# Kernel optimization log

Hardware: AMD Instinct MI355X
Metric: run time of the kernel (lower is better)

## Reference

```python
import jax, jax.numpy as jnp
import numpy as np

B, C, H, W = 16, 512, 64, 64
R = 8
CP = C // R  # inner channel dim C' = 64


def setup_inputs() -> dict:
    key = jax.random.key(0)
    ks = jax.random.split(key, 10)
    s_in = 1.0 / np.sqrt(C)
    s_cp = 1.0 / np.sqrt(CP)
    return {
        "x": jax.random.normal(ks[0], (B, C, H, W), dtype=jnp.float32),
        "wq": jax.random.uniform(ks[1], (CP, C), jnp.float32, -s_in, s_in),
        "bq": jax.random.uniform(ks[2], (CP,), jnp.float32, -s_in, s_in),
        "wk": jax.random.uniform(ks[3], (CP, C), jnp.float32, -s_in, s_in),
        "bk": jax.random.uniform(ks[4], (CP,), jnp.float32, -s_in, s_in),
        "wv": jax.random.uniform(ks[5], (CP, C), jnp.float32, -s_in, s_in),
        "bv": jax.random.uniform(ks[6], (CP,), jnp.float32, -s_in, s_in),
        "wo": jax.random.uniform(ks[7], (C, CP), jnp.float32, -s_cp, s_cp),
        "bo": jax.random.uniform(ks[8], (C,), jnp.float32, -s_cp, s_cp),
        # torch init is gamma=0 (output==x, zero grads to convs); use small
        # nonzero value so the reference exercises the full graph.
        "gamma": jax.random.normal(ks[9], (1,), dtype=jnp.float32) * 0.1,
    }


def reference(x, wq, bq, wk, bk, wv, bv, wo, bo, gamma):
    b, c, h, w = x.shape
    n = h * w
    xf = x.reshape(b, c, n)  # flatten spatial -> (B, C, N)
    # 1x1 convs == channel matmuls
    q = jnp.einsum("oc,bcn->bon", wq, xf) + bq[:, None]  # (B, C', N)
    k = jnp.einsum("oc,bcn->bon", wk, xf) + bk[:, None]  # (B, C', N)
    v = jnp.einsum("oc,bcn->bon", wv, xf) + bv[:, None]  # (B, C', N)
    # energy = bmm(key (B,C',N), query^T (B,N,C')) -> (B, C', C')
    energy = jnp.einsum("bin,bjn->bij", k, q)
    attention = jax.nn.softmax(energy, axis=-1)  # (B, C', C')
    out = jnp.einsum("bij,bjn->bin", attention, v)  # (B, C', N)
    out = jnp.einsum("co,bon->bcn", wo, out) + bo[:, None]  # (B, C, N)
    out = out.reshape(b, c, h, w)
    return gamma * out + x
```

## Files before the change

kernel.cpp:

```cpp
#include <hip/hip_runtime.h>


#define NN 4096
#define CIN 512
#define CPD 64

typedef short s8v __attribute__((ext_vector_type(8)));
typedef float f4v __attribute__((ext_vector_type(4)));
typedef unsigned short u16;

__device__ __forceinline__ u16 f2bf(float f) {
    union { float f; unsigned int u; } c; c.f = f;
    unsigned int r = c.u + 0x7FFFu + ((c.u >> 16) & 1u);
    return (u16)(r >> 16);
}

union PK { uint2 u[2]; s8v v; };

__global__ __launch_bounds__(256) void k_prep(
    const float* __restrict__ wq, const float* __restrict__ wk,
    const float* __restrict__ wv, const float* __restrict__ wo,
    u16* __restrict__ wqkvb, u16* __restrict__ wob)
{
    const int t = blockIdx.x * 256 + threadIdx.x;
    const int i4 = t * 4;
    const float* src; u16* dst; int off;
    if (i4 < 98304) {
        const int r = i4 >> 15;
        src = (r == 0) ? wq : (r == 1) ? wk : wv;
        off = i4 & 32767;
        dst = wqkvb + (r << 15);
    } else {
        src = wo; off = i4 - 98304; dst = wob;
    }
    float4 v = *(const float4*)(src + off);
    u16 tmp[4] = { f2bf(v.x), f2bf(v.y), f2bf(v.z), f2bf(v.w) };
    *(uint2*)(dst + off) = *(const uint2*)tmp;
}

__global__ __launch_bounds__(256, 4) void k_qkv(
    const float* __restrict__ x, const u16* __restrict__ wqkvb,
    const float* __restrict__ bq, const float* __restrict__ bk,
    const float* __restrict__ bv,
    u16* __restrict__ q, u16* __restrict__ k, u16* __restrict__ vt)
{
    const int nb = blockIdx.x, b = blockIdx.y;
    const int t = threadIdx.x;
    const int w = t >> 6, L = t & 63, quad = L >> 4, l15 = L & 15;
    const int n0 = nb * 64;

    __shared__ u16 xs[2][64 * 64];

    const int nl = t & 63, c4b = t >> 6;
    const float* xp = x + (size_t)b * CIN * NN + n0 + nl;

    f4v acc[3][4];
    #pragma unroll
    for (int p = 0; p < 3; ++p)
        #pragma unroll
        for (int nn = 0; nn < 4; ++nn) acc[p][nn] = (f4v){0.f,0.f,0.f,0.f};

    const u16* wb = wqkvb + (size_t)(w * 16 + l15) * CIN;

    float xr[16];
    #pragma unroll
    for (int i = 0; i < 4; ++i)
        #pragma unroll
        for (int j = 0; j < 4; ++j)
            xr[i * 4 + j] = xp[(size_t)((c4b + 4 * i) * 4 + j) * NN];
    #pragma unroll
    for (int i = 0; i < 4; ++i) {
        u16 t4[4];
        #pragma unroll
        for (int j = 0; j < 4; ++j) t4[j] = f2bf(xr[i * 4 + j]);
        const int slot = (c4b + 4 * i) ^ (nl & 15);
        *(uint2*)&xs[0][nl * 64 + slot * 4] = *(const uint2*)t4;
    }
    __syncthreads();

    for (int cc = 0; cc < 8; ++cc) {
        const int buf = cc & 1;
        if (cc < 7) {
            const int c0n = (cc + 1) * 64;
            #pragma unroll
            for (int i = 0; i < 4; ++i)
                #pragma unroll
                for (int j = 0; j < 4; ++j)
                    xr[i * 4 + j] = xp[(size_t)(c0n + (c4b + 4 * i) * 4 + j) * NN];
        }
        #pragma unroll
        for (int ks2 = 0; ks2 < 2; ++ks2) {
            s8v bf[4];
            #pragma unroll
            for (int nn = 0; nn < 4; ++nn) {
                const int row = nn * 16 + l15;
                const int sb = ks2 * 8 + quad * 2;
                PK p_;
                p_.u[0] = *(const uint2*)&xs[buf][row * 64 + ((sb ^ l15) * 4)];
                p_.u[1] = *(const uint2*)&xs[buf][row * 64 + (((sb + 1) ^ l15) * 4)];
                bf[nn] = p_.v;
            }
            const int cgl = cc * 64 + ks2 * 32 + quad * 8;
            #pragma unroll
            for (int p = 0; p < 3; ++p) {
                s8v af = *(const s8v*)(wb + (size_t)p * 64 * CIN + cgl);
                #pragma unroll
                for (int nn = 0; nn < 4; ++nn)
                    acc[p][nn] = __builtin_amdgcn_mfma_f32_16x16x32_bf16(
                        af, bf[nn], acc[p][nn], 0, 0, 0);
            }
        }
        if (cc < 7) {
            #pragma unroll
            for (int i = 0; i < 4; ++i) {
                u16 t4[4];
                #pragma unroll
                for (int j = 0; j < 4; ++j) t4[j] = f2bf(xr[i * 4 + j]);
                const int slot = (c4b + 4 * i) ^ (nl & 15);
                *(uint2*)&xs[buf ^ 1][nl * 64 + slot * 4] = *(const uint2*)t4;
            }
        }
        __syncthreads();
    }

    const int orow = w * 16 + quad * 4;
    {
        float4 q4 = *(const float4*)(bq + orow);
        float4 k4 = *(const float4*)(bk + orow);
        const float qb_[4] = { q4.x, q4.y, q4.z, q4.w };
        const float kb_[4] = { k4.x, k4.y, k4.z, k4.w };
        u16* qp = q + (size_t)b * CPD * NN;
        u16* kp = k + (size_t)b * CPD * NN;
        #pragma unroll
        for (int nn = 0; nn < 4; ++nn) {
            const int n = n0 + nn * 16 + l15;
            #pragma unroll
            for (int r = 0; r < 4; ++r) {
                qp[(size_t)(orow + r) * NN + n] = f2bf(acc[0][nn][r] + qb_[r]);
                kp[(size_t)(orow + r) * NN + n] = f2bf(acc[1][nn][r] + kb_[r]);
            }
        }
    }
    {
        float4 v4 = *(const float4*)(bv + orow);
        const float vb_[4] = { v4.x, v4.y, v4.z, v4.w };
        u16* vtb = vt + (size_t)b * NN * CPD;
        #pragma unroll
        for (int nn = 0; nn < 4; ++nn) {
            const int n = n0 + nn * 16 + l15;
            u16 tmp[4];
            #pragma unroll
            for (int r = 0; r < 4; ++r) tmp[r] = f2bf(acc[2][nn][r] + vb_[r]);
            *(uint2*)(vtb + (size_t)n * CPD + orow) = *(const uint2*)tmp;
        }
    }
}

__global__ __launch_bounds__(256, 4) void k_energy(
    const u16* __restrict__ q, const u16* __restrict__ k,
    float* __restrict__ epart)
{
    const int s = blockIdx.x;
    const int b = blockIdx.y;
    const int t = threadIdx.x;
    const int wv_ = t >> 6, L = t & 63, quad = L >> 4, l15 = L & 15;
    const u16* kb = k + (size_t)b * CPD * NN;
    const u16* qb = q + (size_t)b * CPD * NN;

    f4v acc[4][4];
    #pragma unroll
    for (int a = 0; a < 4; ++a)
        #pragma unroll
        for (int d = 0; d < 4; ++d) acc[a][d] = (f4v){0.f,0.f,0.f,0.f};

    const int nbase = s * 512 + wv_ * 128;
    #pragma unroll
    for (int ksl = 0; ksl < 4; ++ksl) {
        const int n = nbase + ksl * 32 + quad * 8;
        s8v af[4], bf_[4];
        #pragma unroll
        for (int it = 0; it < 4; ++it)
            af[it] = *(const s8v*)(kb + (size_t)(it * 16 + l15) * NN + n);
        #pragma unroll
        for (int jt = 0; jt < 4; ++jt)
            bf_[jt] = *(const s8v*)(qb + (size_t)(jt * 16 + l15) * NN + n);
        #pragma unroll
        for (int it = 0; it < 4; ++it)
            #pragma unroll
            for (int jt = 0; jt < 4; ++jt)
                acc[it][jt] = __builtin_amdgcn_mfma_f32_16x16x32_bf16(
                    af[it], bf_[jt], acc[it][jt], 0, 0, 0);
    }

    float* ep = epart + ((size_t)b * 32 + s * 4 + wv_) * 4096;
    #pragma unroll
    for (int it = 0; it < 4; ++it)
        #pragma unroll
        for (int jt = 0; jt < 4; ++jt)
            #pragma unroll
            for (int r = 0; r < 4; ++r)
                ep[(it * 16 + quad * 4 + r) * 64 + jt * 16 + l15] =
                    acc[it][jt][r];
}

__global__ __launch_bounds__(64) void k_softmax(
    const float* __restrict__ epart, u16* __restrict__ attn)
{
    const int i = blockIdx.x;
    const int b = blockIdx.y;
    const int j = threadIdx.x;
    float s = 0.f;
    #pragma unroll
    for (int sp = 0; sp < 32; ++sp)
        s += epart[((size_t)b * 32 + sp) * 4096 + i * 64 + j];
    float m = s;
    #pragma unroll
    for (int off = 32; off; off >>= 1) m = fmaxf(m, __shfl_xor(m, off));
    float e = __expf(s - m);
    float tot = e;
    #pragma unroll
    for (int off = 32; off; off >>= 1) tot += __shfl_xor(tot, off);
    attn[(size_t)b * 4096 + i * 64 + j] = f2bf(e / tot);
}

__global__ __launch_bounds__(256, 4) void k_avout(
    const u16* __restrict__ vt, const u16* __restrict__ attn,
    const u16* __restrict__ wob, const float* __restrict__ bo,
    const float* __restrict__ gamma, const float* __restrict__ x,
    float* __restrict__ out)
{
    const int nb = blockIdx.x, b = blockIdx.y;
    const int t = threadIdx.x;
    const int wv_ = t >> 6, L = t & 63, quad = L >> 4, l15 = L & 15;
    const int n0 = nb * 64;

    __shared__ u16 avl[64 * 64];

    {
        const u16* ab  = attn + (size_t)b * 4096;
        const u16* vtb = vt + (size_t)b * NN * CPD;
        f4v acc1[4];
        #pragma unroll
        for (int a = 0; a < 4; ++a) acc1[a] = (f4v){0.f,0.f,0.f,0.f};
        const int nloc = wv_ * 16 + l15;
        #pragma unroll
        for (int ks = 0; ks < 2; ++ks) {
            const int j = ks * 32 + quad * 8;
            s8v bfv = *(const s8v*)(vtb + (size_t)(n0 + nloc) * CPD + j);
            #pragma unroll
            for (int it = 0; it < 4; ++it) {
                s8v af = *(const s8v*)(ab + (size_t)(it * 16 + l15) * 64 + j);
                acc1[it] = __builtin_amdgcn_mfma_f32_16x16x32_bf16(
                    af, bfv, acc1[it], 0, 0, 0);
            }
        }
        #pragma unroll
        for (int it = 0; it < 4; ++it) {
            u16 t4[4];
            #pragma unroll
            for (int r = 0; r < 4; ++r) t4[r] = f2bf(acc1[it][r]);
            const int slot = (it * 4 + quad) ^ l15;
            *(uint2*)&avl[nloc * 64 + slot * 4] = *(const uint2*)t4;
        }
    }
    __syncthreads();

    const float g = gamma[0];
    for (int cb = 0; cb < 8; ++cb) {
        f4v acc2[4];
        #pragma unroll
        for (int a = 0; a < 4; ++a) acc2[a] = (f4v){0.f,0.f,0.f,0.f};
        #pragma unroll
        for (int ks = 0; ks < 2; ++ks) {
            const int sb = ks * 8 + quad * 2;
            PK p_;
            p_.u[0] = *(const uint2*)&avl[(wv_ * 16 + l15) * 64 + ((sb ^ l15) * 4)];
            p_.u[1] = *(const uint2*)&avl[(wv_ * 16 + l15) * 64 + (((sb + 1) ^ l15) * 4)];
            const s8v af2 = p_.v;
            const int i0 = ks * 32 + quad * 8;
            #pragma unroll
            for (int ct = 0; ct < 4; ++ct) {
                s8v bf2 = *(const s8v*)(wob +
                    (size_t)(cb * 64 + ct * 16 + l15) * CPD + i0);
                acc2[ct] = __builtin_amdgcn_mfma_f32_16x16x32_bf16(
                    af2, bf2, acc2[ct], 0, 0, 0);
            }
        }
        #pragma unroll
        for (int ct = 0; ct < 4; ++ct) {
            const int c = cb * 64 + ct * 16 + l15;
            const float bs = bo[c];
            const int nb4 = n0 + wv_ * 16 + quad * 4;
            const size_t idx = ((size_t)b * CIN + c) * NN + nb4;
            float4 xr = *(const float4*)(x + idx);
            float4 r4;
            r4.x = g * (acc2[ct][0] + bs) + xr.x;
            r4.y = g * (acc2[ct][1] + bs) + xr.y;
            r4.z = g * (acc2[ct][2] + bs) + xr.z;
            r4.w = g * (acc2[ct][3] + bs) + xr.w;
            *(float4*)(out + idx) = r4;
        }
    }
}

extern "C" void kernel_launch(void* const* d_in, const int* in_sizes, int n_in,
                              void* d_out, int out_size, void* d_ws, size_t ws_size,
                              hipStream_t stream) {
    const float* x  = (const float*)d_in[0];
    const float* wq = (const float*)d_in[1];
    const float* bq = (const float*)d_in[2];
    const float* wk = (const float*)d_in[3];
    const float* bk = (const float*)d_in[4];
    const float* wv = (const float*)d_in[5];
    const float* bv = (const float*)d_in[6];
    const float* wo = (const float*)d_in[7];
    const float* bo = (const float*)d_in[8];
    const float* gm = (const float*)d_in[9];
    float* out = (float*)d_out;

    char* wsb = (char*)d_ws;
    u16*   q     = (u16*)wsb;
    u16*   k     = (u16*)(wsb + 8388608);
    u16*   vt    = (u16*)(wsb + 16777216);
    float* epart = (float*)(wsb + 25165824);
    u16*   attn  = (u16*)(wsb + 33554432);
    u16*   wqkvb = (u16*)(wsb + 33685504);
    u16*   wob   = (u16*)(wsb + 33882112);

    k_prep<<<128, 256, 0, stream>>>(wq, wk, wv, wo, wqkvb, wob);
    k_qkv<<<dim3(64, 16), 256, 0, stream>>>(x, wqkvb, bq, bk, bv, q, k, vt);
    k_energy<<<dim3(8, 16), 256, 0, stream>>>(q, k, epart);
    k_softmax<<<dim3(64, 16), 64, 0, stream>>>(epart, attn);
    k_avout<<<dim3(64, 16), 256, 0, stream>>>(vt, attn, wob, bo, gm, x, out);
}
```

Baseline: 346.6 us.

## Fuse energy computation into QKV kernel via LDS-staged Q/K tiles

The per-tile Q and K results now go into shared memory instead of global memory, and each QKV block computes its partial 64x64 energy directly, writing 64 partials per batch. This removes the separate energy kernel and the global write and re-read of Q and K. The price is twice as much partial-energy traffic, which the softmax kernel must sum over more slices. The x loads in QKV are also software-pipelined two chunks ahead with two register buffers, and the x residual loads in the output kernel are hoisted ahead of the MFMAs.

Measured after the change: 347.4 us. About the same (+0.2%).

```diff
diff --git a/kernel.cpp b/kernel.cpp
--- a/kernel.cpp
+++ b/kernel.cpp
@@ -38,11 +38,11 @@
     *(uint2*)(dst + off) = *(const uint2*)tmp;
 }
 
-__global__ __launch_bounds__(256, 4) void k_qkv(
+__global__ __launch_bounds__(256, 4) void k_qkve(
     const float* __restrict__ x, const u16* __restrict__ wqkvb,
     const float* __restrict__ bq, const float* __restrict__ bk,
     const float* __restrict__ bv,
-    u16* __restrict__ q, u16* __restrict__ k, u16* __restrict__ vt)
+    u16* __restrict__ vt, float* __restrict__ epart)
 {
     const int nb = blockIdx.x, b = blockIdx.y;
     const int t = threadIdx.x;
@@ -62,32 +62,27 @@
 
     const u16* wb = wqkvb + (size_t)(w * 16 + l15) * CIN;
 
-    float xr[16];
-    #pragma unroll
-    for (int i = 0; i < 4; ++i)
-        #pragma unroll
-        for (int j = 0; j < 4; ++j)
-            xr[i * 4 + j] = xp[(size_t)((c4b + 4 * i) * 4 + j) * NN];
-    #pragma unroll
-    for (int i = 0; i < 4; ++i) {
-        u16 t4[4];
-        #pragma unroll
-        for (int j = 0; j < 4; ++j) t4[j] = f2bf(xr[i * 4 + j]);
-        const int slot = (c4b + 4 * i) ^ (nl & 15);
-        *(uint2*)&xs[0][nl * 64 + slot * 4] = *(const uint2*)t4;
-    }
-    __syncthreads();
-
-    for (int cc = 0; cc < 8; ++cc) {
-        const int buf = cc & 1;
-        if (cc < 7) {
-            const int c0n = (cc + 1) * 64;
-            #pragma unroll
-            for (int i = 0; i < 4; ++i)
-                #pragma unroll
-                for (int j = 0; j < 4; ++j)
-                    xr[i * 4 + j] = xp[(size_t)(c0n + (c4b + 4 * i) * 4 + j) * NN];
-        }
+    float xrA[16], xrB[16];
+
+    auto issue = [&](int cc, float* xr) {
+        const int c0n = cc * 64;
+        #pragma unroll
+        for (int i = 0; i < 4; ++i)
+            #pragma unroll
+            for (int j = 0; j < 4; ++j)
+                xr[i * 4 + j] = xp[(size_t)(c0n + (c4b + 4 * i) * 4 + j) * NN];
+    };
+    auto stage = [&](const float* xr, u16* dst) {
+        #pragma unroll
+        for (int i = 0; i < 4; ++i) {
+            u16 t4[4];
+            #pragma unroll
+            for (int j = 0; j < 4; ++j) t4[j] = f2bf(xr[i * 4 + j]);
+            const int slot = (c4b + 4 * i) ^ (nl & 15);
+            *(uint2*)&dst[nl * 64 + slot * 4] = *(const uint2*)t4;
+        }
+    };
+    auto compute = [&](int cc, const u16* src) {
         #pragma unroll
         for (int ks2 = 0; ks2 < 2; ++ks2) {
             s8v bf[4];
@@ -96,8 +91,8 @@
                 const int row = nn * 16 + l15;
                 const int sb = ks2 * 8 + quad * 2;
                 PK p_;
-                p_.u[0] = *(const uint2*)&xs[buf][row * 64 + ((sb ^ l15) * 4)];
-                p_.u[1] = *(const uint2*)&xs[buf][row * 64 + (((sb + 1) ^ l15) * 4)];
+                p_.u[0] = *(const uint2*)&src[row * 64 + ((sb ^ l15) * 4)];
+                p_.u[1] = *(const uint2*)&src[row * 64 + (((sb + 1) ^ l15) * 4)];
                 bf[nn] = p_.v;
             }
             const int cgl = cc * 64 + ks2 * 32 + quad * 8;
@@ -110,97 +105,89 @@
                         af, bf[nn], acc[p][nn], 0, 0, 0);
             }
         }
-        if (cc < 7) {
-            #pragma unroll
-            for (int i = 0; i < 4; ++i) {
-                u16 t4[4];
-                #pragma unroll
-                for (int j = 0; j < 4; ++j) t4[j] = f2bf(xr[i * 4 + j]);
-                const int slot = (c4b + 4 * i) ^ (nl & 15);
-                *(uint2*)&xs[buf ^ 1][nl * 64 + slot * 4] = *(const uint2*)t4;
-            }
-        }
+    };
+
+    issue(0, xrA);
+    issue(1, xrB);
+    stage(xrA, xs[0]);
+    __syncthreads();
+
+    #pragma unroll
+    for (int cb2 = 0; cb2 < 4; ++cb2) {
+        const int cc = cb2 * 2;
+        if (cc + 2 < 8) issue(cc + 2, xrA);
+        compute(cc, xs[0]);
+        stage(xrB, xs[1]);
         __syncthreads();
+        if (cc + 3 < 8) issue(cc + 3, xrB);
+        compute(cc + 1, xs[1]);
+        if (cc + 2 < 8) stage(xrA, xs[0]);
+        __syncthreads();
     }
 
     const int orow = w * 16 + quad * 4;
+
+    {
+        float4 v4 = *(const float4*)(bv + orow);
+        const float vb_[4] = { v4.x, v4.y, v4.z, v4.w };
+        u16* vtb = vt + (size_t)b * NN * CPD;
+        #pragma unroll
+        for (int nn = 0; nn < 4; ++nn) {
+            const int n = n0 + nn * 16 + l15;
+            u16 tmp[4];
+            #pragma unroll
+            for (int r = 0; r < 4; ++r) tmp[r] = f2bf(acc[2][nn][r] + vb_[r]);
+            *(uint2*)(vt + (size_t)b * NN * CPD + (size_t)n * CPD + orow) =
+                *(const uint2*)tmp;
+            (void)vtb;
+        }
+    }
+
+    u16* q_l = &xs[0][0];
+    u16* k_l = &xs[1][0];
     {
         float4 q4 = *(const float4*)(bq + orow);
         float4 k4 = *(const float4*)(bk + orow);
         const float qb_[4] = { q4.x, q4.y, q4.z, q4.w };
         const float kb_[4] = { k4.x, k4.y, k4.z, k4.w };
-        u16* qp = q + (size_t)b * CPD * NN;
-        u16* kp = k + (size_t)b * CPD * NN;
         #pragma unroll
         for (int nn = 0; nn < 4; ++nn) {
-            const int n = n0 + nn * 16 + l15;
+            const int col = nn * 16 + l15;
             #pragma unroll
             for (int r = 0; r < 4; ++r) {
-                qp[(size_t)(orow + r) * NN + n] = f2bf(acc[0][nn][r] + qb_[r]);
-                kp[(size_t)(orow + r) * NN + n] = f2bf(acc[1][nn][r] + kb_[r]);
-            }
-        }
-    }
+                const int row = orow + r;
+                const int cs = col ^ ((row & 7) * 8);
+                q_l[row * 64 + cs] = f2bf(acc[0][nn][r] + qb_[r]);
+                k_l[row * 64 + cs] = f2bf(acc[1][nn][r] + kb_[r]);
+            }
+        }
+    }
+    __syncthreads();
+
     {
-        float4 v4 = *(const float4*)(bv + orow);
-        const float vb_[4] = { v4.x, v4.y, v4.z, v4.w };
-        u16* vtb = vt + (size_t)b * NN * CPD;
-        #pragma unroll
-        for (int nn = 0; nn < 4; ++nn) {
-            const int n = n0 + nn * 16 + l15;
-            u16 tmp[4];
-            #pragma unroll
-            for (int r = 0; r < 4; ++r) tmp[r] = f2bf(acc[2][nn][r] + vb_[r]);
-            *(uint2*)(vtb + (size_t)n * CPD + orow) = *(const uint2*)tmp;
-        }
-    }
-}
-
-__global__ __launch_bounds__(256, 4) void k_energy(
-    const u16* __restrict__ q, const u16* __restrict__ k,
-    float* __restrict__ epart)
-{
-    const int s = blockIdx.x;
-    const int b = blockIdx.y;
-    const int t = threadIdx.x;
-    const int wv_ = t >> 6, L = t & 63, quad = L >> 4, l15 = L & 15;
-    const u16* kb = k + (size_t)b * CPD * NN;
-    const u16* qb = q + (size_t)b * CPD * NN;
-
-    f4v acc[4][4];
-    #pragma unroll
-    for (int a = 0; a < 4; ++a)
-        #pragma unroll
-        for (int d = 0; d < 4; ++d) acc[a][d] = (f4v){0.f,0.f,0.f,0.f};
-
-    const int nbase = s * 512 + wv_ * 128;
-    #pragma unroll
-    for (int ksl = 0; ksl < 4; ++ksl) {
-        const int n = nbase + ksl * 32 + quad * 8;
-        s8v af[4], bf_[4];
-        #pragma unroll
-        for (int it = 0; it < 4; ++it)
-            af[it] = *(const s8v*)(kb + (size_t)(it * 16 + l15) * NN + n);
+        f4v acc_e[4];
+        #pragma unroll
+        for (int jt = 0; jt < 4; ++jt) acc_e[jt] = (f4v){0.f,0.f,0.f,0.f};
+        #pragma unroll
+        for (int ks = 0; ks < 2; ++ks) {
+            const int nsl = ks * 32 + quad * 8;
+            const int arow = w * 16 + l15;
+            s8v afk = *(const s8v*)&k_l[arow * 64 + (nsl ^ ((arow & 7) * 8))];
+            #pragma unroll
+            for (int jt = 0; jt < 4; ++jt) {
+                const int brow = jt * 16 + l15;
+                s8v bfq = *(const s8v*)&q_l[brow * 64 + (nsl ^ ((brow & 7) * 8))];
+                acc_e[jt] = __builtin_amdgcn_mfma_f32_16x16x32_bf16(
+                    afk, bfq, acc_e[jt], 0, 0, 0);
+            }
+        }
+        float* ep = epart + ((size_t)b * 64 + nb) * 4096;
         #pragma unroll
         for (int jt = 0; jt < 4; ++jt)
-            bf_[jt] = *(const s8v*)(qb + (size_t)(jt * 16 + l15) * NN + n);
-        #pragma unroll
-        for (int it = 0; it < 4; ++it)
-            #pragma unroll
-            for (int jt = 0; jt < 4; ++jt)
-                acc[it][jt] = __builtin_amdgcn_mfma_f32_16x16x32_bf16(
-                    af[it], bf_[jt], acc[it][jt], 0, 0, 0);
-    }
-
-    float* ep = epart + ((size_t)b * 32 + s * 4 + wv_) * 4096;
-    #pragma unroll
-    for (int it = 0; it < 4; ++it)
-        #pragma unroll
-        for (int jt = 0; jt < 4; ++jt)
             #pragma unroll
             for (int r = 0; r < 4; ++r)
-                ep[(it * 16 + quad * 4 + r) * 64 + jt * 16 + l15] =
-                    acc[it][jt][r];
+                ep[(w * 16 + quad * 4 + r) * 64 + jt * 16 + l15] = acc_e[jt][r];
+    }
 }
 
 __global__ __launch_bounds__(64) void k_softmax(
@@ -211,8 +198,8 @@
     const int j = threadIdx.x;
     float s = 0.f;
     #pragma unroll
-    for (int sp = 0; sp < 32; ++sp)
-        s += epart[((size_t)b * 32 + sp) * 4096 + i * 64 + j];
+    for (int sp = 0; sp < 64; ++sp)
+        s += epart[((size_t)b * 64 + sp) * 4096 + i * 64 + j];
     float m = s;
     #pragma unroll
     for (int off = 32; off; off >>= 1) m = fmaxf(m, __shfl_xor(m, off));
@@ -267,6 +254,15 @@
 
     const float g = gamma[0];
     for (int cb = 0; cb < 8; ++cb) {
+        float4 xr4[4];
+        size_t idx4[4];
+        #pragma unroll
+        for (int ct = 0; ct < 4; ++ct) {
+            const int c = cb * 64 + ct * 16 + l15;
+            const int nb4 = n0 + wv_ * 16 + quad * 4;
+            idx4[ct] = ((size_t)b * CIN + c) * NN + nb4;
+            xr4[ct] = *(const float4*)(x + idx4[ct]);
+        }
         f4v acc2[4];
         #pragma unroll
         for (int a = 0; a < 4; ++a) acc2[a] = (f4v){0.f,0.f,0.f,0.f};
@@ -288,17 +284,13 @@
         }
         #pragma unroll
         for (int ct = 0; ct < 4; ++ct) {
-            const int c = cb * 64 + ct * 16 + l15;
-            const float bs = bo[c];
-            const int nb4 = n0 + wv_ * 16 + quad * 4;
-            const size_t idx = ((size_t)b * CIN + c) * NN + nb4;
-            float4 xr = *(const float4*)(x + idx);
+            const float bs = bo[cb * 64 + ct * 16 + l15];
             float4 r4;
-            r4.x = g * (acc2[ct][0] + bs) + xr.x;
-            r4.y = g * (acc2[ct][1] + bs) + xr.y;
-            r4.z = g * (acc2[ct][2] + bs) + xr.z;
-            r4.w = g * (acc2[ct][3] + bs) + xr.w;
-            *(float4*)(out + idx) = r4;
+            r4.x = g * (acc2[ct][0] + bs) + xr4[ct].x;
+            r4.y = g * (acc2[ct][1] + bs) + xr4[ct].y;
+            r4.z = g * (acc2[ct][2] + bs) + xr4[ct].z;
+            r4.w = g * (acc2[ct][3] + bs) + xr4[ct].w;
+            *(float4*)(out + idx4[ct]) = r4;
         }
     }
 }
@@ -319,17 +311,14 @@
     float* out = (float*)d_out;
 
     char* wsb = (char*)d_ws;
-    u16*   q     = (u16*)wsb;
-    u16*   k     = (u16*)(wsb + 8388608);
-    u16*   vt    = (u16*)(wsb + 16777216);
-    float* epart = (float*)(wsb + 25165824);
-    u16*   attn  = (u16*)(wsb + 33554432);
-    u16*   wqkvb = (u16*)(wsb + 33685504);
-    u16*   wob   = (u16*)(wsb + 33882112);
+    u16*   vt    = (u16*)wsb;
+    float* epart = (float*)(wsb + 8388608);
+    u16*   attn  = (u16*)(wsb + 25165824);
+    u16*   wqkvb = (u16*)(wsb + 25296896);
+    u16*   wob   = (u16*)(wsb + 25493504);
 
     k_prep<<<128, 256, 0, stream>>>(wq, wk, wv, wo, wqkvb, wob);
-    k_qkv<<<dim3(64, 16), 256, 0, stream>>>(x, wqkvb, bq, bk, bv, q, k, vt);
-    k_energy<<<dim3(8, 16), 256, 0, stream>>>(q, k, epart);
+    k_qkve<<<dim3(64, 16), 256, 0, stream>>>(x, wqkvb, bq, bk, bv, vt, epart);
     k_softmax<<<dim3(64, 16), 64, 0, stream>>>(epart, attn);
     k_avout<<<dim3(64, 16), 256, 0, stream>>>(vt, attn, wob, bo, gm, x, out);
 }
```
